# Optimization experiments

Measured on AMD Instinct MI355X. Metric: run time of the kernel, lower is better.

The kernel has to match this reference:

```python
import jax, jax.numpy as jnp
import numpy as np

N, E, FE, H, G, L, OUT = 50000, 300000, 64, 256, 256, 4, 128
BN_EPS = 1e-5


def setup_inputs() -> dict:
    key = jax.random.key(0)
    ks = jax.random.split(key, 12)
    s = 0.05
    return dict(
        x=jax.random.normal(ks[0], (N, H), jnp.float32),
        edge_index=jax.random.randint(ks[1], (2, E), 0, N, dtype=jnp.int64),
        edge_attr=jax.random.normal(ks[2], (E, FE), jnp.float32),
        batch=jnp.sort(jax.random.randint(ks[3], (N,), 0, G, dtype=jnp.int64)),
        bond_W1=jax.random.normal(ks[4], (L, FE, H), jnp.float32) * s,
        bond_b1=jnp.zeros((L, H), jnp.float32),
        bond_W2=jax.random.normal(ks[5], (L, H, H), jnp.float32) * s,
        bond_b2=jnp.zeros((L, H), jnp.float32),
        mlp_W1=jax.random.normal(ks[6], (L, H, H), jnp.float32) * s,
        mlp_b1=jnp.zeros((L, H), jnp.float32),
        mlp_W2=jax.random.normal(ks[7], (L, H, H), jnp.float32) * s,
        mlp_b2=jnp.zeros((L, H), jnp.float32),
        eps=jnp.zeros((L,), jnp.float32),
        bn_gamma=jnp.ones((L, H), jnp.float32),
        bn_beta=jnp.zeros((L, H), jnp.float32),
        fc1_W=jax.random.normal(ks[8], (L * H, H), jnp.float32) * s,
        fc1_b=jnp.zeros((H,), jnp.float32),
        fc4_W=jax.random.normal(ks[9], (H, OUT), jnp.float32) * s,
        fc4_b=jnp.zeros((OUT,), jnp.float32),
    )


def reference(x, edge_index, edge_attr, batch,
              bond_W1, bond_b1, bond_W2, bond_b2,
              mlp_W1, mlp_b1, mlp_W2, mlp_b2,
              eps, bn_gamma, bn_beta,
              fc1_W, fc1_b, fc4_W, fc4_b):
    src, dst = edge_index[0], edge_index[1]  # x_j gathered from src, scatter-add to dst
    x_lst = []
    for l in range(L):
        # bond encoder: Linear -> ReLU -> Linear on edge features [E, FE] -> [E, H]
        e = jax.nn.relu(edge_attr @ bond_W1[l] + bond_b1[l]) @ bond_W2[l] + bond_b2[l]
        # message = relu(x_j + e), aggregate = scatter-add over destination nodes
        msg = jax.nn.relu(x[src] + e)  # [E, H]
        aggr = jax.ops.segment_sum(msg, dst, num_segments=N)  # [N, H]
        h = (1.0 + eps[l]) * x + aggr
        h = jax.nn.relu(h @ mlp_W1[l] + mlp_b1[l]) @ mlp_W2[l] + mlp_b2[l]
        h = jax.nn.relu(h)
        # BatchNorm over the node dimension (training-style batch statistics)
        mu = jnp.mean(h, axis=0)
        var = jnp.var(h, axis=0)
        x = (h - mu) * jax.lax.rsqrt(var + BN_EPS) * bn_gamma[l] + bn_beta[l]
        x_lst.append(x)
    xc = jnp.concatenate(x_lst, axis=-1)  # [N, L*H]
    # global mean pool over graphs
    sums = jax.ops.segment_sum(xc, batch, num_segments=G)  # [G, L*H]
    cnts = jax.ops.segment_sum(jnp.ones((N,), xc.dtype), batch, num_segments=G)
    pooled = sums / jnp.maximum(cnts, 1.0)[:, None]
    h = jax.nn.relu(pooled @ fc1_W + fc1_b)
    # dropout p=0.5 in eval mode -> identity
    return h @ fc4_W + fc4_b  # [G, OUT]
```

## Files before the change

### kernel.cpp

```cpp
#include <hip/hip_runtime.h>

#define NN 50000
#define NE 300000
#define FEA 64
#define HD 256
#define NG 256
#define NL 4
#define OD 128
#define SCB ((NN + 255) / 256)

typedef unsigned short u16;
typedef unsigned int u32;
typedef __attribute__((ext_vector_type(8))) short short8;
typedef __attribute__((ext_vector_type(4))) short s16x4;
typedef __attribute__((ext_vector_type(4))) float f32x4;

__device__ __forceinline__ u16 f2h(float f) {
    union { _Float16 h; u16 u; } v; v.h = (_Float16)f; return v.u;
}
__device__ __forceinline__ float h2f(u16 u) {
    union { u16 u; _Float16 h; } v; v.u = u; return (float)v.h;
}

typedef const __attribute__((address_space(1))) unsigned int gas_u32;
typedef __attribute__((address_space(3))) unsigned int las_u32;
__device__ __forceinline__ void gld16(const void* g, void* l) {
    __builtin_amdgcn_global_load_lds((gas_u32*)g, (las_u32*)l, 16, 0, 0);
}

__global__ __launch_bounds__(256, 3) void edge_k(
    const u16* __restrict__ eattrS, const u16* __restrict__ W1t,
    const float* __restrict__ bb1, const u16* __restrict__ W2t,
    const float* __restrict__ bb2,
    const int* __restrict__ srcI, const int* __restrict__ dstI,
    const u16* __restrict__ xh, float* __restrict__ aggr)
{
    __shared__ __align__(16) u16 bufT[64 * 256];
    __shared__ __align__(16) u16 bufG[32 * 256];
    __shared__ int srcL[64];
    const int tid = threadIdx.x;
    const int lane = tid & 63;
    const int w = tid >> 6;
    const int q = lane >> 4, c15 = lane & 15;
    const int e0 = blockIdx.x * 64;
    const int wb = tid & ~63;

    if (tid < 64) {
        int er = e0 + tid;
        int erc = er < NE ? er : NE - 1;
        srcL[tid] = srcI[erc];
    }
#pragma unroll
    for (int it = 0; it < 2; ++it) {
        const int i = it * 256 + tid;
        const int m = i >> 3, kb = i & 7;
        int row = e0 + m; if (row > NE - 1) row = NE - 1;
        gld16(eattrS + (size_t)row * FEA + ((kb ^ (m & 7)) * 8),
              &bufT[(it * 256 + wb) * 8]);
    }
    __syncthreads();

#pragma unroll
    for (int it = 0; it < 4; ++it) {
        const int i = it * 256 + tid;
        const int row = i >> 5, ch = i & 31;
        gld16(xh + (size_t)srcL[row] * HD + ch * 8,
              &bufG[(it * 256 + wb) * 8]);
    }

    const u16* w1p[4];
    const u16* w2p[4];
#pragma unroll
    for (int t = 0; t < 4; ++t) {
        const int nn = w * 64 + t * 16 + c15;
        w1p[t] = W1t + (size_t)nn * FEA + q * 8;
        w2p[t] = W2t + (size_t)nn * HD + q * 8;
    }

    f32x4 acc1[4][4];
#pragma unroll
    for (int i = 0; i < 4; ++i)
#pragma unroll
        for (int j = 0; j < 4; ++j) acc1[i][j] = (f32x4)0.0f;
#pragma unroll
    for (int s = 0; s < 2; ++s) {
        short8 af[4], bf[4];
#pragma unroll
        for (int t = 0; t < 4; ++t) {
            const int kga = s * 4 + q;
            const int mm = t * 16 + c15;
            af[t] = *(const short8*)&bufT[mm * 64 + ((kga ^ (mm & 7)) * 8)];
            bf[t] = *(const short8*)(w1p[t] + s * 32);
        }
        __builtin_amdgcn_s_setprio(1);
#pragma unroll
        for (int tm = 0; tm < 4; ++tm)
#pragma unroll
            for (int tn = 0; tn < 4; ++tn)
                acc1[tm][tn] = __builtin_amdgcn_mfma_f32_16x16x32_f16(
                    bf[tm], af[tn], acc1[tm][tn], 0, 0, 0);
        __builtin_amdgcn_s_setprio(0);
    }
    __syncthreads();

    {
#pragma unroll
        for (int tm = 0; tm < 4; ++tm) {
            const float4 b1v = *(const float4*)(bb1 + w * 64 + tm * 16 + q * 4);
            const int kb = w * 8 + tm * 2 + (q >> 1);
#pragma unroll
            for (int tn = 0; tn < 4; ++tn) {
                const int edge = tn * 16 + c15;
                s16x4 o;
#pragma unroll
                for (int r = 0; r < 4; ++r) {
                    float v = acc1[tm][tn][r] + ((const float*)&b1v)[r];
                    v = v > 0.0f ? v : 0.0f;
                    o[r] = (short)f2h(v);
                }
                *(s16x4*)((char*)bufT + edge * 512 +
                          ((kb ^ (edge & 7)) << 4) + ((q & 1) << 3)) = o;
            }
        }
    }
    __syncthreads();

    f32x4 acc2[4][4];
#pragma unroll
    for (int i = 0; i < 4; ++i)
#pragma unroll
        for (int j = 0; j < 4; ++j) acc2[i][j] = (f32x4)0.0f;
#pragma unroll
    for (int c = 0; c < 8; ++c) {
        short8 af[4], bf[4];
#pragma unroll
        for (int t = 0; t < 4; ++t) {
            const int mm = t * 16 + c15;
            const int kbg = c * 4 + q;
            af[t] = *(const short8*)&bufT[mm * 256 + ((kbg ^ (mm & 7)) * 8)];
            bf[t] = *(const short8*)(w2p[t] + c * 32);
        }
        __builtin_amdgcn_s_setprio(1);
#pragma unroll
        for (int tm = 0; tm < 4; ++tm)
#pragma unroll
            for (int tn = 0; tn < 4; ++tn)
                acc2[tm][tn] = __builtin_amdgcn_mfma_f32_16x16x32_f16(
                    af[tm], bf[tn], acc2[tm][tn], 0, 0, 0);
        __builtin_amdgcn_s_setprio(0);
    }

    float b2f[4];
#pragma unroll
    for (int tn = 0; tn < 4; ++tn)
        b2f[tn] = bb2[w * 64 + tn * 16 + c15];
    __syncthreads();

#pragma unroll
    for (int tm = 0; tm < 2; ++tm) {
        const int rc = tm * 2 + (q >> 1);
#pragma unroll
        for (int tn = 0; tn < 4; ++tn) {
            const int col = w * 64 + tn * 16 + c15;
            s16x4 o;
#pragma unroll
            for (int r = 0; r < 4; ++r) {
                const int row = tm * 16 + q * 4 + r;
                float v = acc2[tm][tn][r] + b2f[tn]
                        + h2f(bufG[row * 256 + col]);
                v = v > 0.0f ? v : 0.0f;
                o[r] = (short)f2h(v);
            }
            *(s16x4*)((char*)bufT + col * 128 +
                      ((rc ^ (col & 7)) << 4) + ((q & 1) << 3)) = o;
        }
    }
    __syncthreads();

#pragma unroll
    for (int it = 0; it < 4; ++it) {
        const int i = it * 256 + tid;
        const int row = 32 + (i >> 5), ch = i & 31;
        gld16(xh + (size_t)srcL[row] * HD + ch * 8,
              &bufG[(it * 256 + wb) * 8]);
    }
    __syncthreads();

#pragma unroll
    for (int tm = 2; tm < 4; ++tm) {
        const int rc = tm * 2 + (q >> 1);
#pragma unroll
        for (int tn = 0; tn < 4; ++tn) {
            const int col = w * 64 + tn * 16 + c15;
            s16x4 o;
#pragma unroll
            for (int r = 0; r < 4; ++r) {
                const int rowG = (tm - 2) * 16 + q * 4 + r;
                float v = acc2[tm][tn][r] + b2f[tn]
                        + h2f(bufG[rowG * 256 + col]);
                v = v > 0.0f ? v : 0.0f;
                o[r] = (short)f2h(v);
            }
            *(s16x4*)((char*)bufT + col * 128 +
                      ((rc ^ (col & 7)) << 4) + ((q & 1) << 3)) = o;
        }
    }
    __syncthreads();

    {
        const char* bT = (const char*)bufT;
        float s = 0.0f;
        int cur = dstI[e0];
#pragma unroll
        for (int j = 0; j < 8; ++j) {
            short8 m8 = *(const short8*)(bT + tid * 128 + ((j ^ (tid & 7)) << 4));
#pragma unroll
            for (int si = 0; si < 8; ++si) {
                const int er = e0 + j * 8 + si;
                const int d = (er < NE) ? dstI[er] : -1;
                if (d != cur) {
                    if (cur >= 0 && s != 0.0f)
                        unsafeAtomicAdd(&aggr[(size_t)cur * HD + tid], s);
                    cur = d; s = 0.0f;
                }
                s += h2f((u16)m8[si]);
            }
        }
        if (cur >= 0 && s != 0.0f)
            unsafeAtomicAdd(&aggr[(size_t)cur * HD + tid], s);
    }
}

__global__ __launch_bounds__(256, 4) void node_k(
    const u16* __restrict__ xh, const float* __restrict__ aggr,
    const float* __restrict__ epsv, int l,
    const u16* __restrict__ M1t, const float* __restrict__ mb1,
    const u16* __restrict__ M2t, const float* __restrict__ mb2,
    u16* __restrict__ hb, float* __restrict__ bns, float* __restrict__ bnq)
{
    __shared__ __align__(16) u16 bufT[64 * 256];
    const int tid = threadIdx.x;
    const int lane = tid & 63;
    const int w = tid >> 6;
    const int q = lane >> 4, c15 = lane & 15;
    const int n0b = blockIdx.x * 64;
    const float e1 = 1.0f + epsv[l];

    const u16* m1p[4];
    const u16* m2p[4];
#pragma unroll
    for (int t = 0; t < 4; ++t) {
        const int nn = w * 64 + t * 16 + c15;
        m1p[t] = M1t + (size_t)nn * HD + q * 8;
        m2p[t] = M2t + (size_t)nn * HD + q * 8;
    }

#pragma unroll
    for (int it = 0; it < 8; ++it) {
        const int i = it * 256 + tid;
        const int m = i >> 5, kb = i & 31;
        int row = n0b + m; if (row > NN - 1) row = NN - 1;
        const size_t base = (size_t)row * HD + kb * 8;
        short8 xv = *(const short8*)(xh + base);
        float4 a0 = *(const float4*)(aggr + base);
        float4 a1 = *(const float4*)(aggr + base + 4);
        u16 o[8];
        o[0] = f2h(e1 * h2f((u16)xv[0]) + a0.x);
        o[1] = f2h(e1 * h2f((u16)xv[1]) + a0.y);
        o[2] = f2h(e1 * h2f((u16)xv[2]) + a0.z);
        o[3] = f2h(e1 * h2f((u16)xv[3]) + a0.w);
        o[4] = f2h(e1 * h2f((u16)xv[4]) + a1.x);
        o[5] = f2h(e1 * h2f((u16)xv[5]) + a1.y);
        o[6] = f2h(e1 * h2f((u16)xv[6]) + a1.z);
        o[7] = f2h(e1 * h2f((u16)xv[7]) + a1.w);
        *(short8*)&bufT[m * 256 + ((kb ^ (m & 7)) * 8)] = *(short8*)o;
    }
    __syncthreads();

    f32x4 acc1[4][4];
#pragma unroll
    for (int i = 0; i < 4; ++i)
#pragma unroll
        for (int j = 0; j < 4; ++j) acc1[i][j] = (f32x4)0.0f;
#pragma unroll
    for (int c = 0; c < 8; ++c) {
        short8 af[4], bf[4];
#pragma unroll
        for (int t = 0; t < 4; ++t) {
            const int mm = t * 16 + c15;
            const int kbg = c * 4 + q;
            af[t] = *(const short8*)&bufT[mm * 256 + ((kbg ^ (mm & 7)) * 8)];
            bf[t] = *(const short8*)(m1p[t] + c * 32);
        }
        __builtin_amdgcn_s_setprio(1);
#pragma unroll
        for (int tm = 0; tm < 4; ++tm)
#pragma unroll
            for (int tn = 0; tn < 4; ++tn)
                acc1[tm][tn] = __builtin_amdgcn_mfma_f32_16x16x32_f16(
                    bf[tm], af[tn], acc1[tm][tn], 0, 0, 0);
        __builtin_amdgcn_s_setprio(0);
    }
    __syncthreads();

    {
#pragma unroll
        for (int tm = 0; tm < 4; ++tm) {
            const float4 b1v = *(const float4*)(mb1 + w * 64 + tm * 16 + q * 4);
            const int kb = w * 8 + tm * 2 + (q >> 1);
#pragma unroll
            for (int tn = 0; tn < 4; ++tn) {
                const int node = tn * 16 + c15;
                s16x4 o;
#pragma unroll
                for (int r = 0; r < 4; ++r) {
                    float v = acc1[tm][tn][r] + ((const float*)&b1v)[r];
                    v = v > 0.0f ? v : 0.0f;
                    o[r] = (short)f2h(v);
                }
                *(s16x4*)((char*)bufT + node * 512 +
                          ((kb ^ (node & 7)) << 4) + ((q & 1) << 3)) = o;
            }
        }
    }
    __syncthreads();

    f32x4 acc2[4][4];
#pragma unroll
    for (int i = 0; i < 4; ++i)
#pragma unroll
        for (int j = 0; j < 4; ++j) acc2[i][j] = (f32x4)0.0f;
#pragma unroll
    for (int c = 0; c < 8; ++c) {
        short8 af[4], bf[4];
#pragma unroll
        for (int t = 0; t < 4; ++t) {
            const int mm = t * 16 + c15;
            const int kbg = c * 4 + q;
            af[t] = *(const short8*)&bufT[mm * 256 + ((kbg ^ (mm & 7)) * 8)];
            bf[t] = *(const short8*)(m2p[t] + c * 32);
        }
        __builtin_amdgcn_s_setprio(1);
#pragma unroll
        for (int tm = 0; tm < 4; ++tm)
#pragma unroll
            for (int tn = 0; tn < 4; ++tn)
                acc2[tm][tn] = __builtin_amdgcn_mfma_f32_16x16x32_f16(
                    af[tm], bf[tn], acc2[tm][tn], 0, 0, 0);
        __builtin_amdgcn_s_setprio(0);
    }

    float b2f[4];
#pragma unroll
    for (int tn = 0; tn < 4; ++tn)
        b2f[tn] = mb2[w * 64 + tn * 16 + c15];
    float ps[4] = {0, 0, 0, 0}, pq[4] = {0, 0, 0, 0};
#pragma unroll
    for (int tm = 0; tm < 4; ++tm) {
#pragma unroll
        for (int r = 0; r < 4; ++r) {
            const int grow = n0b + tm * 16 + q * 4 + r;
            if (grow < NN) {
#pragma unroll
                for (int tn = 0; tn < 4; ++tn) {
                    const int col = w * 64 + tn * 16 + c15;
                    float v = acc2[tm][tn][r] + b2f[tn];
                    v = v > 0.0f ? v : 0.0f;
                    hb[(size_t)grow * HD + col] = f2h(v);
                    ps[tn] += v; pq[tn] += v * v;
                }
            }
        }
    }
#pragma unroll
    for (int tn = 0; tn < 4; ++tn) {
        float s = ps[tn], sq = pq[tn];
        s += __shfl_down(s, 32, 64);  sq += __shfl_down(sq, 32, 64);
        s += __shfl_down(s, 16, 64);  sq += __shfl_down(sq, 16, 64);
        if (q == 0) {
            const int col = w * 64 + tn * 16 + c15;
            unsafeAtomicAdd(&bns[col], s);
            unsafeAtomicAdd(&bnq[col], sq);
        }
    }
}


__global__ void transpose_k(const float* __restrict__ in, u16* __restrict__ oh,
                            int Kw, int Nw) {
    int i = blockIdx.x * blockDim.x + threadIdx.x;
    int tot = NL * Kw * Nw;
    if (i < tot) {
        int l = i / (Kw * Nw), rem = i % (Kw * Nw);
        int k = rem / Nw, n = rem % Nw;
        oh[(size_t)l * Kw * Nw + (size_t)n * Kw + k] = f2h(in[i]);
    }
}

__global__ void cvt_k(const float* __restrict__ in, u16* __restrict__ outh, int tot) {
    int i = blockIdx.x * blockDim.x + threadIdx.x;
    if (i < tot) outh[i] = f2h(in[i]);
}

__global__ void egather_k(const float* __restrict__ eattr, const int* __restrict__ perm,
                          u16* __restrict__ eattrS) {
    int i = blockIdx.x * blockDim.x + threadIdx.x;
    if (i < NE * FEA) {
        int row = i >> 6, k = i & 63;
        eattrS[i] = f2h(eattr[(size_t)perm[row] * FEA + k]);
    }
}

__global__ void zero_layer_k(float4* __restrict__ aggr4, float* __restrict__ bns,
                             float* __restrict__ bnq) {
    int i = blockIdx.x * blockDim.x + threadIdx.x;
    if (i < (NN * HD) / 4) aggr4[i] = make_float4(0.f, 0.f, 0.f, 0.f);
    if (i < HD) { bns[i] = 0.0f; bnq[i] = 0.0f; }
}

__global__ void zerof_k(float* __restrict__ p, int n) {
    int i = blockIdx.x * blockDim.x + threadIdx.x;
    if (i < n) p[i] = 0.0f;
}

__global__ void bnfin_k(const float* __restrict__ bns, const float* __restrict__ bnq,
                        const float* __restrict__ gamma, const float* __restrict__ beta,
                        int l, float* __restrict__ ab) {
    int c = threadIdx.x;
    float mu = bns[c] * (1.0f / (float)NN);
    float var = bnq[c] * (1.0f / (float)NN) - mu * mu;
    if (var < 0.0f) var = 0.0f;
    float a = gamma[l * HD + c] * rsqrtf(var + 1e-5f);
    float b = beta[l * HD + c] - mu * a;
    ab[c] = a; ab[HD + c] = b;
}

__global__ void bnapply_k(const u16* __restrict__ hb, const float* __restrict__ ab,
                          const int* __restrict__ batch, u16* __restrict__ xh,
                          float* __restrict__ pooled, int l) {
    const int t = threadIdx.x;
    const int n0 = blockIdx.x * 64;
    const float a = ab[t], b = ab[HD + t];
    const int hi = (NN - n0 < 64) ? (NN - n0) : 64;
    float s = 0.0f;
    int cur = batch[n0];
    for (int r = 0; r < hi; ++r) {
        const size_t idx = (size_t)(n0 + r) * HD + t;
        float v = a * h2f(hb[idx]) + b;
        xh[idx] = f2h(v);
        const int g = batch[n0 + r];
        if (g != cur) {
            unsafeAtomicAdd(&pooled[(size_t)cur * (NL * HD) + l * HD + t], s);
            s = 0.0f; cur = g;
        }
        s += v;
    }
    unsafeAtomicAdd(&pooled[(size_t)cur * (NL * HD) + l * HD + t], s);
}


__global__ void zeroi_k(int* __restrict__ a, int n) {
    int i = blockIdx.x * blockDim.x + threadIdx.x;
    if (i < n) a[i] = 0;
}

__global__ void hist_k(const int* __restrict__ dst, int* __restrict__ hist) {
    int e = blockIdx.x * blockDim.x + threadIdx.x;
    if (e < NE) atomicAdd(&hist[dst[e]], 1);
}

__global__ void sumblk_k(const int* __restrict__ hist, int* __restrict__ psum) {
    __shared__ int red[256];
    int b = blockIdx.x, t = threadIdx.x, i = b * 256 + t;
    red[t] = (i < NN) ? hist[i] : 0;
    __syncthreads();
    for (int o = 128; o > 0; o >>= 1) {
        if (t < o) red[t] += red[t + o];
        __syncthreads();
    }
    if (t == 0) psum[b] = red[0];
}

__global__ void scanblk_k(int* __restrict__ psum) {
    __shared__ int sc[256];
    int t = threadIdx.x;
    int v = (t < SCB) ? psum[t] : 0;
    sc[t] = v; __syncthreads();
    for (int o = 1; o < 256; o <<= 1) {
        int x = (t >= o) ? sc[t - o] : 0;
        __syncthreads(); sc[t] += x; __syncthreads();
    }
    if (t < SCB) psum[t] = sc[t] - v;
}

__global__ void scanfin_k(const int* __restrict__ hist, const int* __restrict__ psum,
                          int* __restrict__ rowptr) {
    __shared__ int sc[256];
    int b = blockIdx.x, t = threadIdx.x, i = b * 256 + t;
    int v = (i < NN) ? hist[i] : 0;
    sc[t] = v; __syncthreads();
    for (int o = 1; o < 256; o <<= 1) {
        int x = (t >= o) ? sc[t - o] : 0;
        __syncthreads(); sc[t] += x; __syncthreads();
    }
    if (i < NN) rowptr[i] = psum[b] + sc[t] - v;
    if (i == NN - 1) rowptr[NN] = psum[b] + sc[t];
}

__global__ void copyi_k(const int* __restrict__ src, int* __restrict__ dst, int n) {
    int i = blockIdx.x * blockDim.x + threadIdx.x;
    if (i < n) dst[i] = src[i];
}

__global__ void scatter_k(const int* __restrict__ dst, int* __restrict__ next,
                          int* __restrict__ perm) {
    int e = blockIdx.x * blockDim.x + threadIdx.x;
    if (e < NE) {
        int p = atomicAdd(&next[dst[e]], 1);
        perm[p] = e;
    }
}

__global__ void permsd_k(const int* __restrict__ eidx, const int* __restrict__ perm,
                         int* __restrict__ srcS, int* __restrict__ dstS) {
    int i = blockIdx.x * blockDim.x + threadIdx.x;
    if (i < NE) {
        int e = perm[i];
        srcS[i] = eidx[e];
        dstS[i] = eidx[NE + e];
    }
}


__global__ void zcnt_k(int* __restrict__ cnts) {
    if (threadIdx.x < NG) cnts[threadIdx.x] = 0;
}

__global__ void count_k(const int* __restrict__ batch, int* __restrict__ cnts) {
    int i = blockIdx.x * blockDim.x + threadIdx.x;
    if (i < NN) atomicAdd(&cnts[batch[i]], 1);
}

__global__ void fc_k(const float* __restrict__ pooled, const int* __restrict__ cnts,
                     const float* __restrict__ W1, const float* __restrict__ b1,
                     const float* __restrict__ W4, const float* __restrict__ b4,
                     float* __restrict__ out) {
    __shared__ float pl[NL * HD];
    __shared__ float hm[HD];
    int g = blockIdx.x, t = threadIdx.x;
    const float inv = 1.0f / fmaxf((float)cnts[g], 1.0f);
#pragma unroll
    for (int j = 0; j < 4; ++j)
        pl[t + j * 256] = pooled[(size_t)g * 1024 + t + j * 256] * inv;
    __syncthreads();
    float a = b1[t];
    for (int k = 0; k < 1024; ++k) a += pl[k] * W1[k * 256 + t];
    hm[t] = a > 0.0f ? a : 0.0f;
    __syncthreads();
    if (t < OD) {
        float o = b4[t];
        for (int k = 0; k < 256; ++k) o += hm[k] * W4[k * OD + t];
        out[g * OD + t] = o;
    }
}


extern "C" void kernel_launch(void* const* d_in, const int* in_sizes, int n_in,
                              void* d_out, int out_size, void* d_ws, size_t ws_size,
                              hipStream_t stream) {
    const float* x_in  = (const float*)d_in[0];
    const int*   eidx  = (const int*)d_in[1];
    const float* eattr = (const float*)d_in[2];
    const int*   batch = (const int*)d_in[3];
    const float* bW1   = (const float*)d_in[4];
    const float* bb1   = (const float*)d_in[5];
    const float* bW2   = (const float*)d_in[6];
    const float* bb2   = (const float*)d_in[7];
    const float* mW1   = (const float*)d_in[8];
    const float* mb1   = (const float*)d_in[9];
    const float* mW2   = (const float*)d_in[10];
    const float* mb2   = (const float*)d_in[11];
    const float* epsv  = (const float*)d_in[12];
    const float* gamma = (const float*)d_in[13];
    const float* beta  = (const float*)d_in[14];
    const float* fc1W  = (const float*)d_in[15];
    const float* fc1b  = (const float*)d_in[16];
    const float* fc4W  = (const float*)d_in[17];
    const float* fc4b  = (const float*)d_in[18];
    float* out = (float*)d_out;
    (void)in_sizes; (void)n_in; (void)out_size; (void)ws_size;

    size_t off = 0;
    auto alloc = [&](size_t bytes) -> char* {
        char* r = (char*)d_ws + off;
        off = (off + bytes + 255) & ~(size_t)255;
        return r;
    };
    u16*   xh   = (u16*)alloc((size_t)NN * HD * 2);
    float* aggr = (float*)alloc((size_t)NN * HD * 4);
    u16*   hb   = (u16*)alloc((size_t)NN * HD * 2);
    u16*   eattrS = (u16*)alloc((size_t)NE * FEA * 2);
    u16*   W1t  = (u16*)alloc((size_t)NL * FEA * HD * 2);
    u16*   W2t  = (u16*)alloc((size_t)NL * HD * HD * 2);
    u16*   M1t  = (u16*)alloc((size_t)NL * HD * HD * 2);
    u16*   M2t  = (u16*)alloc((size_t)NL * HD * HD * 2);
    float* bns  = (float*)alloc(HD * 4);
    float* bnq  = (float*)alloc(HD * 4);
    float* ab   = (float*)alloc(2 * HD * 4);
    int*   cnts = (int*)alloc(NG * 4);
    float* pooled = (float*)alloc((size_t)NG * NL * HD * 4);
    int*   hist  = (int*)alloc((size_t)NN * 4);
    int*   psum  = (int*)alloc((size_t)SCB * 4);
    int*   rowptr = (int*)alloc((size_t)(NN + 1) * 4);
    int*   perm  = (int*)alloc((size_t)NE * 4);
    int*   srcS  = (int*)alloc((size_t)NE * 4);
    int*   dstS  = (int*)alloc((size_t)NE * 4);

    const int NEL = NN * HD;
    const int EB = (NEL + 255) / 256;
    const int EB4 = (NEL / 4 + 255) / 256;
    const int NEB = (NE + 255) / 256;

    transpose_k<<<(NL * FEA * HD + 255) / 256, 256, 0, stream>>>(bW1, W1t, FEA, HD);
    transpose_k<<<(NL * HD * HD + 255) / 256, 256, 0, stream>>>(bW2, W2t, HD, HD);
    transpose_k<<<(NL * HD * HD + 255) / 256, 256, 0, stream>>>(mW1, M1t, HD, HD);
    transpose_k<<<(NL * HD * HD + 255) / 256, 256, 0, stream>>>(mW2, M2t, HD, HD);

    cvt_k<<<EB, 256, 0, stream>>>(x_in, xh, NEL);

    zeroi_k<<<(NN + 255) / 256, 256, 0, stream>>>(hist, NN);
    hist_k<<<NEB, 256, 0, stream>>>(eidx + NE, hist);
    sumblk_k<<<SCB, 256, 0, stream>>>(hist, psum);
    scanblk_k<<<1, 256, 0, stream>>>(psum);
    scanfin_k<<<SCB, 256, 0, stream>>>(hist, psum, rowptr);
    copyi_k<<<(NN + 255) / 256, 256, 0, stream>>>(rowptr, hist, NN);
    scatter_k<<<NEB, 256, 0, stream>>>(eidx + NE, hist, perm);
    permsd_k<<<NEB, 256, 0, stream>>>(eidx, perm, srcS, dstS);
    egather_k<<<(NE * FEA + 255) / 256, 256, 0, stream>>>(eattr, perm, eattrS);

    zcnt_k<<<1, 256, 0, stream>>>(cnts);
    count_k<<<(NN + 255) / 256, 256, 0, stream>>>(batch, cnts);
    zerof_k<<<(NG * NL * HD + 255) / 256, 256, 0, stream>>>(pooled, NG * NL * HD);

    const int EGB = (NE + 63) / 64;
    const int NGB = (NN + 63) / 64;

    for (int l = 0; l < NL; ++l) {
        zero_layer_k<<<EB4, 256, 0, stream>>>((float4*)aggr, bns, bnq);
        edge_k<<<EGB, 256, 0, stream>>>(
            eattrS, W1t + (size_t)l * FEA * HD, bb1 + l * HD,
            W2t + (size_t)l * HD * HD, bb2 + l * HD,
            srcS, dstS, xh, aggr);
        node_k<<<NGB, 256, 0, stream>>>(
            xh, aggr, epsv, l,
            M1t + (size_t)l * HD * HD, mb1 + l * HD,
            M2t + (size_t)l * HD * HD, mb2 + l * HD,
            hb, bns, bnq);
        bnfin_k<<<1, HD, 0, stream>>>(bns, bnq, gamma, beta, l, ab);
        bnapply_k<<<NGB, 256, 0, stream>>>(hb, ab, batch, xh, pooled, l);
    }
    fc_k<<<NG, 256, 0, stream>>>(pooled, cnts, fc1W, fc1b, fc4W, fc4b, out);
}
```

Measured before the change: 1.389 ms.

## Prefetch weight fragments and gather all source rows up front in edge kernel

In the edge kernel, the full 64-row x[src] gather now goes into a doubled, XOR-swizzled LDS buffer in one pass. This removes the mid-epilogue reload and its extra barriers. The kernel also preloads the W1 fragments and software-pipelines the W2 fragment loads one K-chunk ahead. The node kernel gets the same double-buffered weight prefetch, including prefetching the first M2 chunk during the M1 loop. The trade-off is more LDS and registers per block, so edge_k's launch bound drops from 3 to 2 blocks per CU, which lowers occupancy.

```diff
diff --git a/kernel.cpp b/kernel.cpp
--- a/kernel.cpp
+++ b/kernel.cpp
@@ -28,7 +28,7 @@
     __builtin_amdgcn_global_load_lds((gas_u32*)g, (las_u32*)l, 16, 0, 0);
 }
 
-__global__ __launch_bounds__(256, 3) void edge_k(
+__global__ __launch_bounds__(256, 2) void edge_k(
     const u16* __restrict__ eattrS, const u16* __restrict__ W1t,
     const float* __restrict__ bb1, const u16* __restrict__ W2t,
     const float* __restrict__ bb2,
@@ -36,7 +36,7 @@
     const u16* __restrict__ xh, float* __restrict__ aggr)
 {
     __shared__ __align__(16) u16 bufT[64 * 256];
-    __shared__ __align__(16) u16 bufG[32 * 256];
+    __shared__ __align__(16) u16 bufG[64 * 256];
     __shared__ int srcL[64];
     const int tid = threadIdx.x;
     const int lane = tid & 63;
@@ -60,14 +60,6 @@
     }
     __syncthreads();
 
-#pragma unroll
-    for (int it = 0; it < 4; ++it) {
-        const int i = it * 256 + tid;
-        const int row = i >> 5, ch = i & 31;
-        gld16(xh + (size_t)srcL[row] * HD + ch * 8,
-              &bufG[(it * 256 + wb) * 8]);
-    }
-
     const u16* w1p[4];
     const u16* w2p[4];
 #pragma unroll
@@ -76,6 +68,24 @@
         w1p[t] = W1t + (size_t)nn * FEA + q * 8;
         w2p[t] = W2t + (size_t)nn * HD + q * 8;
     }
+    short8 b1f[2][4];
+#pragma unroll
+    for (int s = 0; s < 2; ++s)
+#pragma unroll
+        for (int t = 0; t < 4; ++t)
+            b1f[s][t] = *(const short8*)(w1p[t] + s * 32);
+    short8 bfc[4], bfn[4];
+#pragma unroll
+    for (int t = 0; t < 4; ++t)
+        bfc[t] = *(const short8*)(w2p[t]);
+
+#pragma unroll
+    for (int it = 0; it < 8; ++it) {
+        const int i = it * 256 + tid;
+        const int row = i >> 5, chs = i & 31;
+        gld16(xh + (size_t)srcL[row] * HD + ((chs ^ (row & 7)) * 8),
+              &bufG[(it * 256 + wb) * 8]);
+    }
 
     f32x4 acc1[4][4];
 #pragma unroll
@@ -84,13 +94,12 @@
         for (int j = 0; j < 4; ++j) acc1[i][j] = (f32x4)0.0f;
 #pragma unroll
     for (int s = 0; s < 2; ++s) {
-        short8 af[4], bf[4];
+        short8 af[4];
 #pragma unroll
         for (int t = 0; t < 4; ++t) {
             const int kga = s * 4 + q;
             const int mm = t * 16 + c15;
             af[t] = *(const short8*)&bufT[mm * 64 + ((kga ^ (mm & 7)) * 8)];
-            bf[t] = *(const short8*)(w1p[t] + s * 32);
         }
         __builtin_amdgcn_s_setprio(1);
 #pragma unroll
@@ -98,7 +107,7 @@
 #pragma unroll
             for (int tn = 0; tn < 4; ++tn)
                 acc1[tm][tn] = __builtin_amdgcn_mfma_f32_16x16x32_f16(
-                    bf[tm], af[tn], acc1[tm][tn], 0, 0, 0);
+                    b1f[s][tm], af[tn], acc1[tm][tn], 0, 0, 0);
         __builtin_amdgcn_s_setprio(0);
     }
     __syncthreads();
@@ -132,13 +141,17 @@
         for (int j = 0; j < 4; ++j) acc2[i][j] = (f32x4)0.0f;
 #pragma unroll
     for (int c = 0; c < 8; ++c) {
-        short8 af[4], bf[4];
+        if (c < 7) {
+#pragma unroll
+            for (int t = 0; t < 4; ++t)
+                bfn[t] = *(const short8*)(w2p[t] + (c + 1) * 32);
+        }
+        short8 af[4];
 #pragma unroll
         for (int t = 0; t < 4; ++t) {
             const int mm = t * 16 + c15;
             const int kbg = c * 4 + q;
             af[t] = *(const short8*)&bufT[mm * 256 + ((kbg ^ (mm & 7)) * 8)];
-            bf[t] = *(const short8*)(w2p[t] + c * 32);
         }
         __builtin_amdgcn_s_setprio(1);
 #pragma unroll
@@ -146,8 +159,12 @@
 #pragma unroll
             for (int tn = 0; tn < 4; ++tn)
                 acc2[tm][tn] = __builtin_amdgcn_mfma_f32_16x16x32_f16(
-                    af[tm], bf[tn], acc2[tm][tn], 0, 0, 0);
+                    af[tm], bfc[tn], acc2[tm][tn], 0, 0, 0);
         __builtin_amdgcn_s_setprio(0);
+        if (c < 7) {
+#pragma unroll
+            for (int t = 0; t < 4; ++t) bfc[t] = bfn[t];
+        }
     }
 
     float b2f[4];
@@ -157,7 +174,7 @@
     __syncthreads();
 
 #pragma unroll
-    for (int tm = 0; tm < 2; ++tm) {
+    for (int tm = 0; tm < 4; ++tm) {
         const int rc = tm * 2 + (q >> 1);
 #pragma unroll
         for (int tn = 0; tn < 4; ++tn) {
@@ -166,38 +183,9 @@
 #pragma unroll
             for (int r = 0; r < 4; ++r) {
                 const int row = tm * 16 + q * 4 + r;
-                float v = acc2[tm][tn][r] + b2f[tn]
-                        + h2f(bufG[row * 256 + col]);
-                v = v > 0.0f ? v : 0.0f;
-                o[r] = (short)f2h(v);
-            }
-            *(s16x4*)((char*)bufT + col * 128 +
-                      ((rc ^ (col & 7)) << 4) + ((q & 1) << 3)) = o;
-        }
-    }
-    __syncthreads();
-
-#pragma unroll
-    for (int it = 0; it < 4; ++it) {
-        const int i = it * 256 + tid;
-        const int row = 32 + (i >> 5), ch = i & 31;
-        gld16(xh + (size_t)srcL[row] * HD + ch * 8,
-              &bufG[(it * 256 + wb) * 8]);
-    }
-    __syncthreads();
-
-#pragma unroll
-    for (int tm = 2; tm < 4; ++tm) {
-        const int rc = tm * 2 + (q >> 1);
-#pragma unroll
-        for (int tn = 0; tn < 4; ++tn) {
-            const int col = w * 64 + tn * 16 + c15;
-            s16x4 o;
-#pragma unroll
-            for (int r = 0; r < 4; ++r) {
-                const int rowG = (tm - 2) * 16 + q * 4 + r;
-                float v = acc2[tm][tn][r] + b2f[tn]
-                        + h2f(bufG[rowG * 256 + col]);
+                const u16 xv = bufG[row * 256 +
+                                    ((((col >> 3) ^ (row & 7)) << 3)) + (col & 7)];
+                float v = acc2[tm][tn][r] + b2f[tn] + h2f(xv);
                 v = v > 0.0f ? v : 0.0f;
                 o[r] = (short)f2h(v);
             }
@@ -246,14 +234,10 @@
     const int n0b = blockIdx.x * 64;
     const float e1 = 1.0f + epsv[l];
 
-    const u16* m1p[4];
-    const u16* m2p[4];
-#pragma unroll
-    for (int t = 0; t < 4; ++t) {
+    auto wfrag = [&](const u16* base, int t, int cc) -> short8 {
         const int nn = w * 64 + t * 16 + c15;
-        m1p[t] = M1t + (size_t)nn * HD + q * 8;
-        m2p[t] = M2t + (size_t)nn * HD + q * 8;
-    }
+        return *(const short8*)(base + (size_t)nn * HD + q * 8 + cc * 32);
+    };
 
 #pragma unroll
     for (int it = 0; it < 8; ++it) {
@@ -275,6 +259,9 @@
         o[7] = f2h(e1 * h2f((u16)xv[7]) + a1.w);
         *(short8*)&bufT[m * 256 + ((kb ^ (m & 7)) * 8)] = *(short8*)o;
     }
+    short8 bfc[4], bfn[4];
+#pragma unroll
+    for (int t = 0; t < 4; ++t) bfc[t] = wfrag(M1t, t, 0);
     __syncthreads();
 
     f32x4 acc1[4][4];
@@ -284,13 +271,15 @@
         for (int j = 0; j < 4; ++j) acc1[i][j] = (f32x4)0.0f;
 #pragma unroll
     for (int c = 0; c < 8; ++c) {
-        short8 af[4], bf[4];
+#pragma unroll
+        for (int t = 0; t < 4; ++t)
+            bfn[t] = (c < 7) ? wfrag(M1t, t, c + 1) : wfrag(M2t, t, 0);
+        short8 af[4];
 #pragma unroll
         for (int t = 0; t < 4; ++t) {
             const int mm = t * 16 + c15;
             const int kbg = c * 4 + q;
             af[t] = *(const short8*)&bufT[mm * 256 + ((kbg ^ (mm & 7)) * 8)];
-            bf[t] = *(const short8*)(m1p[t] + c * 32);
         }
         __builtin_amdgcn_s_setprio(1);
 #pragma unroll
@@ -298,8 +287,10 @@
 #pragma unroll
             for (int tn = 0; tn < 4; ++tn)
                 acc1[tm][tn] = __builtin_amdgcn_mfma_f32_16x16x32_f16(
-                    bf[tm], af[tn], acc1[tm][tn], 0, 0, 0);
+                    bfc[tm], af[tn], acc1[tm][tn], 0, 0, 0);
         __builtin_amdgcn_s_setprio(0);
+#pragma unroll
+        for (int t = 0; t < 4; ++t) bfc[t] = bfn[t];
     }
     __syncthreads();
 
@@ -332,13 +323,16 @@
         for (int j = 0; j < 4; ++j) acc2[i][j] = (f32x4)0.0f;
 #pragma unroll
     for (int c = 0; c < 8; ++c) {
-        short8 af[4], bf[4];
+        if (c < 7) {
+#pragma unroll
+            for (int t = 0; t < 4; ++t) bfn[t] = wfrag(M2t, t, c + 1);
+        }
+        short8 af[4];
 #pragma unroll
         for (int t = 0; t < 4; ++t) {
             const int mm = t * 16 + c15;
             const int kbg = c * 4 + q;
             af[t] = *(const short8*)&bufT[mm * 256 + ((kbg ^ (mm & 7)) * 8)];
-            bf[t] = *(const short8*)(m2p[t] + c * 32);
         }
         __builtin_amdgcn_s_setprio(1);
 #pragma unroll
@@ -346,8 +340,12 @@
 #pragma unroll
             for (int tn = 0; tn < 4; ++tn)
                 acc2[tm][tn] = __builtin_amdgcn_mfma_f32_16x16x32_f16(
-                    af[tm], bf[tn], acc2[tm][tn], 0, 0, 0);
+                    af[tm], bfc[tn], acc2[tm][tn], 0, 0, 0);
         __builtin_amdgcn_s_setprio(0);
+        if (c < 7) {
+#pragma unroll
+            for (int t = 0; t < 4; ++t) bfc[t] = bfn[t];
+        }
     }
 
     float b2f[4];
```

New measurement: 1.373 ms. About the same (-1.2%).
